# Optimization experiments

Measured on AMD Instinct MI355X. Metric: run time of the kernel, lower is better.

## Reference

```python
import jax, jax.numpy as jnp
import numpy as np

B, T, C, H, W = 4, 5, 512, 32, 32   # bt = B*T = 20
G = 32                              # GroupNorm groups
EPS = 1e-6


def group_norm(x, gamma, beta):
    # x: [N, C, H, W]; normalize per (group-channels, H, W)
    n, c, h, w = x.shape
    xg = x.reshape(n, G, c // G, h * w)
    mu = jnp.mean(xg, axis=(2, 3), keepdims=True)
    var = jnp.mean((xg - mu) ** 2, axis=(2, 3), keepdims=True)
    xn = ((xg - mu) * jax.lax.rsqrt(var + EPS)).reshape(n, c, h, w)
    return xn * gamma[None, :, None, None] + beta[None, :, None, None]


def conv1x1(x, w, b):
    # 1x1 conv == channel matmul. x: [N,C,H,W], w: [O,C], b: [O]
    return jnp.einsum('nchw,oc->nohw', x, w) + b[None, :, None, None]


def setup_inputs() -> dict:
    key = jax.random.key(0)
    ks = jax.random.split(key, 9)
    inp = {'x': jax.random.normal(ks[0], (B * T, C, H, W), jnp.float32)}
    for i, nm in enumerate(['wq', 'wk', 'wv', 'wo', 'wqt', 'wkt', 'wvt', 'wot']):
        inp[nm] = jax.random.normal(ks[i + 1], (C, C), jnp.float32) * 0.02
        inp['b' + nm[1:]] = jnp.zeros((C,), jnp.float32)
    inp['gamma_s'] = jnp.ones((C,), jnp.float32)
    inp['beta_s'] = jnp.zeros((C,), jnp.float32)
    inp['gamma_t'] = jnp.ones((C,), jnp.float32)
    inp['beta_t'] = jnp.zeros((C,), jnp.float32)
    return inp


def reference(x, wq, bq, wk, bk, wv, bv, wo, bo,
              wqt, bqt, wkt, bkt, wvt, bvt, wot, bot,
              gamma_s, beta_s, gamma_t, beta_t):
    scale = float(C) ** -0.5

    # ---- spatial attention (AttnBlock.forward) ----
    hn = group_norm(x, gamma_s, beta_s)
    q = conv1x1(hn, wq, bq).reshape(B * T, C, H * W)
    k = conv1x1(hn, wk, bk).reshape(B * T, C, H * W)
    v = conv1x1(hn, wv, bv).reshape(B * T, C, H * W)
    # scores [bt, hw_q, hw_k], softmax over keys
    att = jax.nn.softmax(jnp.einsum('bcq,bck->bqk', q, k) * scale, axis=2)
    hsp = jnp.einsum('bck,bqk->bcq', v, att).reshape(B * T, C, H, W)
    spatio = x + conv1x1(hsp, wo, bo)

    # ---- temporal attention across t=5 frames per pixel ----
    hn = group_norm(spatio, gamma_t, beta_t)
    q5 = conv1x1(hn, wqt, bqt).reshape(B, T, C, H, W)
    k5 = conv1x1(hn, wkt, bkt).reshape(B, T, C, H, W)
    v5 = conv1x1(hn, wvt, bvt).reshape(B, T, C, H, W)
    # per-pixel [t, t] attention, softmax over key-frame axis s
    att_t = jax.nn.softmax(jnp.einsum('btchw,bschw->bhwts', q5, k5) * scale, axis=-1)
    htp = jnp.einsum('bhwts,bschw->btchw', att_t, v5).reshape(B * T, C, H, W)

    # NOTE: residual is the ORIGINAL x (faithful to the source), not spatio
    return x + conv1x1(htp, wot, bot)
```

## Files before the change

kernel.cpp:

```cpp
#include <hip/hip_runtime.h>
#include <hip/hip_bf16.h>
#include <stdint.h>

typedef unsigned short u16;
typedef __attribute__((ext_vector_type(8))) short bf16x8;
typedef __attribute__((ext_vector_type(4))) float f32x4;

#define DI __device__ __forceinline__

DI float b2f(u16 u) { return __uint_as_float(((uint32_t)u) << 16); }
DI u16 f2b(float f) {
  uint32_t u = __float_as_uint(f);
  u += 0x7fff + ((u >> 16) & 1);
  return (u16)(u >> 16);
}

DI void gld_lds16(const u16* g, u16* l) {
  __builtin_amdgcn_global_load_lds((const __attribute__((address_space(1))) void*)g,
                                   (__attribute__((address_space(3))) void*)l,
                                   16, 0, 0);
}

__global__ __launch_bounds__(256)
void prep(const float* __restrict__ x, const float* __restrict__ gamma,
          const float* __restrict__ beta, u16* __restrict__ gnout,
          const float* __restrict__ w0, const float* __restrict__ w1,
          const float* __restrict__ w2, const float* __restrict__ w3,
          const float* __restrict__ w4, const float* __restrict__ w5,
          const float* __restrict__ w6, const float* __restrict__ w7,
          const float* __restrict__ b0, const float* __restrict__ b1,
          const float* __restrict__ b2, const float* __restrict__ b3,
          const float* __restrict__ b4, const float* __restrict__ b5,
          const float* __restrict__ b6, const float* __restrict__ b7,
          u16* __restrict__ dst, float* __restrict__ bdst)
{
  const int t = threadIdx.x;
  if (blockIdx.x < 640) {
    const int w = (blockIdx.x & 7) * 80 + (blockIdx.x >> 3);
    const int n = w >> 5, g = w & 31;
    const int C = 512, HW = 1024;
    const float* xg = x + ((long)n * C + g * 16) * HW;
    float s = 0.f, ss = 0.f;
    for (int ch = t; ch < 4096; ch += 256) {
      float4 u = *(const float4*)(xg + ch * 4);
      s += u.x + u.y + u.z + u.w;
      ss += u.x * u.x + u.y * u.y + u.z * u.z + u.w * u.w;
    }
#pragma unroll
    for (int off = 32; off > 0; off >>= 1) { s += __shfl_xor(s, off); ss += __shfl_xor(ss, off); }
    __shared__ float rs[4], rss[4];
    if ((t & 63) == 0) { rs[t >> 6] = s; rss[t >> 6] = ss; }
    __syncthreads();
    s  = rs[0] + rs[1] + rs[2] + rs[3];
    ss = rss[0] + rss[1] + rss[2] + rss[3];
    const float mu = s * (1.f / 16384.f);
    const float var = ss * (1.f / 16384.f) - mu * mu;
    const float rstd = rsqrtf(var + 1e-6f);
    float gm[16], bt[16];
#pragma unroll
    for (int i = 0; i < 16; ++i) {
      float ga = gamma[g * 16 + i];
      gm[i] = ga * rstd;
      bt[i] = beta[g * 16 + i] - mu * ga * rstd;
    }
    for (int p = t; p < 1024; p += 256) {
      alignas(16) u16 vals[16];
#pragma unroll
      for (int i = 0; i < 16; ++i)
        vals[i] = f2b(xg[(long)i * HW + p] * gm[i] + bt[i]);
      u16* dp = gnout + ((long)n * HW + p) * C + g * 16;
      *(uint4*)dp       = *(const uint4*)&vals[0];
      *(uint4*)(dp + 8) = *(const uint4*)&vals[8];
    }
    return;
  }
  const int sb = blockIdx.x - 640;
  if (sb >= 1036) {
    bdst[8192 + (sb - 1036) * 256 + t] = 0.f;
    return;
  }
  if (sb >= 1034) {
    const int a = (sb - 1034) * 256 + t;
    float acc = 0.f;
    for (int c = 0; c < 512; ++c) acc += w7[a * 512 + c] * b6[c];
    bdst[4608 + a] = acc + b7[a];
    return;
  }
  if (sb >= 1032) {
    const int a = (sb - 1032) * 256 + t;
    float acc = 0.f;
    for (int c = 0; c < 512; ++c) acc += w3[a * 512 + c] * b2[c];
    bdst[4096 + a] = acc;
    return;
  }
  if (sb >= 1024) {
    const float* bs8[8] = {b0, b1, b2, b3, b4, b5, b6, b7};
    const int a = sb - 1024;
    bdst[a * 512 + t] = bs8[a][t];
    bdst[a * 512 + t + 256] = bs8[a][t + 256];
    return;
  }
  const float* srcs[8] = {w0, w1, w2, w3, w4, w5, w6, w7};
  const int mat = sb >> 7;
  const int i = (((sb & 127) << 8) + t) * 8;
  const float* s = srcs[mat];
  float4 a = *(const float4*)(s + i);
  float4 b = *(const float4*)(s + i + 4);
  alignas(16) u16 v[8] = {f2b(a.x), f2b(a.y), f2b(a.z), f2b(a.w),
                          f2b(b.x), f2b(b.y), f2b(b.z), f2b(b.w)};
  *(uint4*)(dst + (long)mat * 262144 + i) = *(const uint4*)v;
  if (mat == 2 || mat == 6) {
    const int slot = (mat == 2) ? 8 : 10;
    const int row = i >> 9, col = i & 511;
#pragma unroll
    for (int j = 0; j < 8; ++j) dst[(long)slot * 262144 + (col + j) * 512 + row] = v[j];
  }
}

template<int OUTF32, int BIASMODE, int RESID, int SMEXP, int COLSCALE>
DI void gemm_body(const u16* __restrict__ Ab, long lda,
                  const u16* __restrict__ Bb, long ldb,
                  void* __restrict__ C, long cb,
                  const float* __restrict__ bias,
                  const float* __restrict__ resid, long rb,
                  int N, int K, float alpha,
                  float* __restrict__ stats, long stb,
                  int m0, int n0, u16* lA, u16* lB)
{
  const int t = threadIdx.x;
  const int lane = t & 63;
  const int wid = t >> 6;
  const int row = t >> 2;
  const int kc  = (((t & 3) ^ ((t >> 3) & 3)) << 3);

  f32x4 acc[4][4];
#pragma unroll
  for (int i = 0; i < 4; ++i)
#pragma unroll
    for (int j = 0; j < 4; ++j) acc[i][j] = (f32x4){0.f, 0.f, 0.f, 0.f};

  const int ml = lane & 15, qd = lane >> 4;
  const int koff = ((qd ^ ((ml >> 1) & 3)) << 3);
  const int wm = (wid >> 1) * 64, wn = (wid & 1) * 64;

  auto stage = [&](int bsel, int k0) {
    const u16* Ap = Ab + (long)(m0 + row) * lda + (k0 + kc);
    const u16* Bp = Bb + (long)(n0 + row) * ldb + (k0 + kc);
    u16* la = lA + bsel * 4096 + wid * 512;
    u16* lb = lB + bsel * 4096 + wid * 512;
    gld_lds16(Ap, la);
    gld_lds16(Ap + 64 * lda, la + 2048);
    gld_lds16(Bp, lb);
    gld_lds16(Bp + 64 * ldb, lb + 2048);
  };

  const int niter = K >> 5;
  stage(0, 0);
  for (int i = 0; i < niter; ++i) {
    __syncthreads();
    if (i + 1 < niter) stage((i + 1) & 1, (i + 1) << 5);
    const u16* la = lA + (i & 1) * 4096;
    const u16* lb = lB + (i & 1) * 4096;
    bf16x8 af[4], bfr[4];
#pragma unroll
    for (int x = 0; x < 4; ++x)
      af[x] = *(const bf16x8*)&la[(wm + x * 16 + ml) * 32 + koff];
#pragma unroll
    for (int y = 0; y < 4; ++y)
      bfr[y] = *(const bf16x8*)&lb[(wn + y * 16 + ml) * 32 + koff];
#pragma unroll
    for (int x = 0; x < 4; ++x)
#pragma unroll
      for (int y = 0; y < 4; ++y)
        acc[x][y] = __builtin_amdgcn_mfma_f32_16x16x32_bf16(af[x], bfr[y], acc[x][y], 0, 0, 0);
  }

  float inv[4], bcol[4];
  if (COLSCALE) {
#pragma unroll
    for (int j = 0; j < 4; ++j)
      inv[j] = 1.f / stats[stb + n0 + wn + j * 16 + ml];
  }
  if (BIASMODE == 2) {
#pragma unroll
    for (int j = 0; j < 4; ++j) bcol[j] = bias[n0 + wn + j * 16 + ml];
  }
  if (SMEXP) {
    float rs[16];
#pragma unroll
    for (int s = 0; s < 16; ++s) rs[s] = 0.f;
#pragma unroll
    for (int i = 0; i < 4; ++i)
#pragma unroll
      for (int j = 0; j < 4; ++j)
#pragma unroll
        for (int r2 = 0; r2 < 4; ++r2) {
          float e = __expf(acc[i][j][r2] * alpha);
          acc[i][j][r2] = e;
          rs[i * 4 + r2] += e;
        }
#pragma unroll
    for (int m = 1; m < 16; m <<= 1)
#pragma unroll
      for (int s = 0; s < 16; ++s) rs[s] += __shfl_xor(rs[s], m);
    if (ml == 0) {
#pragma unroll
      for (int i = 0; i < 4; ++i)
#pragma unroll
        for (int r2 = 0; r2 < 4; ++r2)
          atomicAdd(&stats[stb + m0 + wm + i * 16 + qd * 4 + r2], rs[i * 4 + r2]);
    }
  }

#pragma unroll
  for (int i = 0; i < 4; ++i) {
#pragma unroll
    for (int r2 = 0; r2 < 4; ++r2) {
      const int rr = m0 + wm + i * 16 + qd * 4 + r2;
      const float brow = (BIASMODE == 1) ? bias[rr] : 0.f;
      const long base = (long)rr * N + n0 + wn + ml;
#pragma unroll
      for (int j = 0; j < 4; ++j) {
        float v = acc[i][j][r2];
        if (!SMEXP) v *= alpha;
        if (COLSCALE) v *= inv[j];
        if (BIASMODE == 1) v += brow;
        if (BIASMODE == 2) v += bcol[j];
        const long ix = base + j * 16;
        if (RESID) v += resid[rb + ix];
        if (OUTF32) ((float*)C)[cb + ix] = v;
        else        ((u16*)C)[cb + ix] = f2b(v);
      }
    }
  }
}

template<int OUTF32, int BIASMODE, int RESID, int SMEXP, int COLSCALE>
__global__ __launch_bounds__(256)
void gemm_bt(const u16* __restrict__ A, long sA, long lda,
             const u16* __restrict__ B, long sB, long ldb,
             void* __restrict__ C, long sC,
             const float* __restrict__ bias,
             const float* __restrict__ resid, long sR,
             int N, int K, float alpha, float* __restrict__ stats)
{
  __shared__ u16 lA[2 * 128 * 32];
  __shared__ u16 lB[2 * 128 * 32];
  const uint32_t nx = gridDim.x, ny = gridDim.y;
  const uint32_t tpz = nx * ny;
  const uint32_t nblk = tpz * gridDim.z;
  const uint32_t g = ((uint32_t)blockIdx.z * ny + blockIdx.y) * nx + blockIdx.x;
  const uint32_t idx = (g & 7u) * (nblk >> 3) + (g >> 3);
  const uint32_t bz = idx / tpz;
  const uint32_t r   = idx - bz * tpz;
  const int m0 = (int)(r / nx) * 128, n0 = (int)(r % nx) * 128;
  gemm_body<OUTF32, BIASMODE, RESID, SMEXP, COLSCALE>(
      A + bz * sA, lda, B + bz * sB, ldb, C, bz * sC, bias, resid, bz * sR,
      N, K, alpha, stats, (long)bz * 1024, m0, n0, lA, lB);
}

__global__ __launch_bounds__(256)
void gemm_qkvv(const u16* __restrict__ hn, const u16* __restrict__ Wqk,
               u16* __restrict__ qkout, const float* __restrict__ bqk,
               const u16* __restrict__ Wov, u16* __restrict__ vvout,
               const float* __restrict__ bvv)
{
  __shared__ u16 lA[2 * 128 * 32];
  __shared__ u16 lB[2 * 128 * 32];
  const long S = 524288;
  const uint32_t g = blockIdx.x;
  if (g < 1280) {
    const uint32_t idx = (g & 7u) * 160 + (g >> 3);
    const int m0 = (int)(idx >> 3) * 128, n0 = (int)(idx & 7u) * 128;
    gemm_body<0, 2, 0, 0, 0>(hn, 512, Wqk, 512, qkout, 0, bqk, nullptr, 0,
                             1024, 512, 1.f, nullptr, 0, m0, n0, lA, lB);
  } else {
    const uint32_t gg = g - 1280;
    const uint32_t idx = (gg & 7u) * 80 + (gg >> 3);
    const uint32_t bz = idx >> 5;
    const uint32_t r = idx & 31u;
    const int m0 = (int)(r >> 3) * 128, n0 = (int)(r & 7u) * 128;
    gemm_body<0, 1, 0, 0, 0>(Wov, 512, hn + (long)bz * S, 512, vvout,
                             (long)bz * S, bvv, nullptr, 0,
                             1024, 512, 1.f, nullptr, 0, m0, n0, lA, lB);
  }
}

__global__ __launch_bounds__(256)
void groupnorm_resid(const u16* __restrict__ h, const float* __restrict__ x,
                     const float* __restrict__ gamma,
                     const float* __restrict__ beta, u16* __restrict__ out)
{
  const int C = 512, HW = 1024;
  const int w = (blockIdx.x & 7) * 80 + (blockIdx.x >> 3);
  const int n = w >> 5, g = w & 31;
  const long base = ((long)n * C + g * 16) * HW;
  const float* xg = x + base;
  const u16*  hg = h + base;
  const int t = threadIdx.x;
  float s = 0.f, ss = 0.f;
  for (int ch = t; ch < 4096; ch += 256) {
    float4 u = *(const float4*)(xg + ch * 4);
    uint2 hv = *(const uint2*)(hg + ch * 4);
    float h0 = __uint_as_float(hv.x << 16);
    float h1 = __uint_as_float(hv.x & 0xffff0000u);
    float h2 = __uint_as_float(hv.y << 16);
    float h3 = __uint_as_float(hv.y & 0xffff0000u);
    float v0 = u.x + h0, v1 = u.y + h1, v2 = u.z + h2, v3 = u.w + h3;
    s += v0 + v1 + v2 + v3;
    ss += v0 * v0 + v1 * v1 + v2 * v2 + v3 * v3;
  }
#pragma unroll
  for (int off = 32; off > 0; off >>= 1) { s += __shfl_xor(s, off); ss += __shfl_xor(ss, off); }
  __shared__ float rs[4], rss[4];
  if ((t & 63) == 0) { rs[t >> 6] = s; rss[t >> 6] = ss; }
  __syncthreads();
  s  = rs[0] + rs[1] + rs[2] + rs[3];
  ss = rss[0] + rss[1] + rss[2] + rss[3];
  const float mu = s * (1.f / 16384.f);
  const float var = ss * (1.f / 16384.f) - mu * mu;
  const float rstd = rsqrtf(var + 1e-6f);
  float gm[16], bt[16];
#pragma unroll
  for (int i = 0; i < 16; ++i) {
    float ga = gamma[g * 16 + i];
    gm[i] = ga * rstd;
    bt[i] = beta[g * 16 + i] - mu * ga * rstd;
  }
  for (int p = t; p < 1024; p += 256) {
    alignas(16) u16 vals[16];
#pragma unroll
    for (int i = 0; i < 16; ++i)
      vals[i] = f2b((xg[(long)i * HW + p] + b2f(hg[(long)i * HW + p])) * gm[i] + bt[i]);
    u16* dst = out + ((long)n * HW + p) * C + g * 16;
    *(uint4*)dst       = *(const uint4*)&vals[0];
    *(uint4*)(dst + 8) = *(const uint4*)&vals[8];
  }
}

__global__ __launch_bounds__(256)
void temporal_attn(const u16* __restrict__ qk, const u16* __restrict__ hn,
                   u16* __restrict__ htp)
{
  const int t = threadIdx.x;
  const int wv = t >> 6, lane = t & 63;
  const int pix = blockIdx.x * 4 + wv;
  const int b = pix >> 10, p = pix & 1023;
  const long fsq = 1024l * 1024;
  const long rowq = ((long)b * 5 * 1024 + p) * 1024 + lane * 8;
  const long fsh = 1024l * 512;
  const long rowh = ((long)b * 5 * 1024 + p) * 512 + lane * 8;

  float qf[5][8], kf[5][8];
#pragma unroll
  for (int f = 0; f < 5; ++f) {
    bf16x8 qv = *(const bf16x8*)(qk + rowq + f * fsq);
    bf16x8 kv = *(const bf16x8*)(qk + rowq + f * fsq + 512);
#pragma unroll
    for (int u = 0; u < 8; ++u) { qf[f][u] = b2f((u16)qv[u]); kf[f][u] = b2f((u16)kv[u]); }
  }
  float sc[25];
#pragma unroll
  for (int i = 0; i < 5; ++i)
#pragma unroll
    for (int j = 0; j < 5; ++j) {
      float a = 0.f;
#pragma unroll
      for (int u = 0; u < 8; ++u) a += qf[i][u] * kf[j][u];
      sc[i * 5 + j] = a;
    }
#pragma unroll
  for (int m = 1; m < 64; m <<= 1)
#pragma unroll
    for (int s = 0; s < 25; ++s) sc[s] += __shfl_xor(sc[s], m);

  const float scale = 0.04419417382415922f;
  float att[5][5];
#pragma unroll
  for (int i = 0; i < 5; ++i) {
    float m = sc[i * 5];
#pragma unroll
    for (int j = 1; j < 5; ++j) m = fmaxf(m, sc[i * 5 + j]);
    float ssum = 0.f;
#pragma unroll
    for (int j = 0; j < 5; ++j) { att[i][j] = __expf((sc[i * 5 + j] - m) * scale); ssum += att[i][j]; }
    float inv = 1.f / ssum;
#pragma unroll
    for (int j = 0; j < 5; ++j) att[i][j] *= inv;
  }

  float of[5][8];
#pragma unroll
  for (int i = 0; i < 5; ++i)
#pragma unroll
    for (int u = 0; u < 8; ++u) of[i][u] = 0.f;
#pragma unroll
  for (int s = 0; s < 5; ++s) {
    bf16x8 vvv = *(const bf16x8*)(hn + rowh + s * fsh);
#pragma unroll
    for (int u = 0; u < 8; ++u) {
      float vf = b2f((u16)vvv[u]);
#pragma unroll
      for (int i = 0; i < 5; ++i) of[i][u] += att[i][s] * vf;
    }
  }
#pragma unroll
  for (int i = 0; i < 5; ++i) {
    alignas(16) u16 ob[8];
#pragma unroll
    for (int u = 0; u < 8; ++u) ob[u] = f2b(of[i][u]);
    *(uint4*)(htp + rowh + i * fsh) = *(const uint4*)ob;
  }
}

extern "C" void kernel_launch(void* const* d_in, const int* in_sizes, int n_in,
                              void* d_out, int out_size, void* d_ws, size_t ws_size,
                              hipStream_t stream)
{
  const float* x   = (const float*)d_in[0];
  const float* wq  = (const float*)d_in[1];
  const float* bq  = (const float*)d_in[2];
  const float* wk  = (const float*)d_in[3];
  const float* bk  = (const float*)d_in[4];
  const float* wv  = (const float*)d_in[5];
  const float* bv  = (const float*)d_in[6];
  const float* wo  = (const float*)d_in[7];
  const float* bo  = (const float*)d_in[8];
  const float* wqt = (const float*)d_in[9];
  const float* bqt = (const float*)d_in[10];
  const float* wkt = (const float*)d_in[11];
  const float* bkt = (const float*)d_in[12];
  const float* wvt = (const float*)d_in[13];
  const float* bvt = (const float*)d_in[14];
  const float* wot = (const float*)d_in[15];
  const float* bot = (const float*)d_in[16];
  const float* gs  = (const float*)d_in[17];
  const float* bs  = (const float*)d_in[18];
  const float* gt  = (const float*)d_in[19];
  const float* btt = (const float*)d_in[20];

  const long U = 20l * 1024 * 512;
  u16* W0 = (u16*)d_ws;
  u16* W1 = W0 + U;
  u16* W3 = W0 + 3 * U;
  u16* W4 = W0 + 4 * U;
  u16* W6 = W0 + 6 * U;
  u16* W7 = W0 + 7 * U;
  u16* Wt = W0 + 8 * U;
  u16* wvT_b  = Wt + 8 * 262144;
  u16* Wovs   = Wt + 9 * 262144;
  u16* Wovt_b = Wt + 11 * 262144;
  float* Bf = (float*)(Wt + 12 * 262144);
  float* Stats = Bf + 8192;
  u16* wo_b  = Wt + 3 * 262144;
  u16* wqt_b = Wt + 4 * 262144;

  const long S  = 524288;
  const long S2 = 1048576;
  const float scale = 0.04419417382415922f;
  dim3 blk(256);

  prep<<<1756, blk, 0, stream>>>(x, gs, bs, W0,
                                 wq, wk, wv, wo, wqt, wkt, wvt, wot,
                                 bq, bk, bv, bo, bqt, bkt, bvt, bot, Wt, Bf);

  gemm_bt<0, 0, 0, 0, 0><<<dim3(4, 4, 2), blk, 0, stream>>>(
      wo_b, 4 * 262144, 512, wvT_b, 2 * 262144, 512, Wovs, 2 * 262144,
      nullptr, nullptr, 0, 512, 512, 1.f, nullptr);

  gemm_qkvv<<<1920, blk, 0, stream>>>(W0, Wt, W1, Bf, Wovs, W3, Bf + 4096);

  gemm_bt<0, 0, 0, 1, 0><<<dim3(8, 8, 20), blk, 0, stream>>>(
      W1, S2, 1024, W1 + 512, S2, 1024, W4, S2, nullptr, nullptr, 0, 1024, 512, scale, Stats);
  gemm_bt<0, 1, 0, 0, 1><<<dim3(8, 4, 20), blk, 0, stream>>>(
      W3, S, 1024, W4, S2, 1024, W6, S, Bf + 1536, nullptr, 0, 1024, 1024, 1.f, Stats);
  groupnorm_resid<<<640, blk, 0, stream>>>(W6, x, gt, btt, W7);
  gemm_bt<0, 2, 0, 0, 0><<<dim3(8, 160, 1), blk, 0, stream>>>(
      W7, 0, 512, wqt_b, 0, 512, W1, 0, Bf + 2048, nullptr, 0, 1024, 512, 1.f, nullptr);
  temporal_attn<<<1024, blk, 0, stream>>>(W1, W7, W0);
  gemm_bt<1, 1, 1, 0, 0><<<dim3(8, 4, 20), blk, 0, stream>>>(
      Wovt_b, 0, 512, W0, S, 512, (float*)d_out, S, Bf + 4608, x, S, 1024, 512, 1.f, nullptr);
}
```

Measured before the change: 390.4 us.

## Fold Wq/Wk into a single bilinear matrix for spatial and temporal scores

Replaces separate Q and K projections with one projection by a precomputed Wq^T·Wk product, so scores become hn·(M·hn) plus a key-side bias term from Wk^T·bq. The query-side bias terms cancel under the row softmax and are dropped. This halves the projection GEMM output width for both attention stages, and temporal attention reuses hn as both query and value inputs. The cost is an extra small weight-product GEMM, per-row bias dot products, and a modest change in bf16 rounding behaviour.

```diff
diff --git a/kernel.cpp b/kernel.cpp
--- a/kernel.cpp
+++ b/kernel.cpp
@@ -75,8 +75,22 @@
     return;
   }
   const int sb = blockIdx.x - 640;
+  if (sb >= 1040) {
+    bdst[8192 + (sb - 1040) * 256 + t] = 0.f;
+    return;
+  }
+  if (sb >= 1038) {
+    const int d = (sb - 1038) * 256 + t;
+    float acc = 0.f;
+    for (int e = 0; e < 512; ++e) acc += w5[(long)e * 512 + d] * b4[e];
+    bdst[5632 + d] = acc;
+    return;
+  }
   if (sb >= 1036) {
-    bdst[8192 + (sb - 1036) * 256 + t] = 0.f;
+    const int d = (sb - 1036) * 256 + t;
+    float acc = 0.f;
+    for (int e = 0; e < 512; ++e) acc += w1[(long)e * 512 + d] * b0[e];
+    bdst[5120 + d] = acc;
     return;
   }
   if (sb >= 1034) {
@@ -109,15 +123,16 @@
   alignas(16) u16 v[8] = {f2b(a.x), f2b(a.y), f2b(a.z), f2b(a.w),
                           f2b(b.x), f2b(b.y), f2b(b.z), f2b(b.w)};
   *(uint4*)(dst + (long)mat * 262144 + i) = *(const uint4*)v;
-  if (mat == 2 || mat == 6) {
-    const int slot = (mat == 2) ? 8 : 10;
+  const int tmap[8] = {11, 16, 8, -1, 15, 20, 12, -1};
+  const int ts = tmap[mat];
+  if (ts >= 0) {
     const int row = i >> 9, col = i & 511;
 #pragma unroll
-    for (int j = 0; j < 8; ++j) dst[(long)slot * 262144 + (col + j) * 512 + row] = v[j];
-  }
-}
-
-template<int OUTF32, int BIASMODE, int RESID, int SMEXP, int COLSCALE>
+    for (int j = 0; j < 8; ++j) dst[(long)ts * 262144 + (col + j) * 512 + row] = v[j];
+  }
+}
+
+template<int OUTF32, int BIASMODE, int RESID, int SMEXP, int COLSCALE, int COLB>
 DI void gemm_body(const u16* __restrict__ Ab, long lda,
                   const u16* __restrict__ Bb, long ldb,
                   void* __restrict__ C, long cb,
@@ -125,6 +140,7 @@
                   const float* __restrict__ resid, long rb,
                   int N, int K, float alpha,
                   float* __restrict__ stats, long stb,
+                  const float* __restrict__ cbias, long cbb,
                   int m0, int n0, u16* lA, u16* lB)
 {
   const int t = threadIdx.x;
@@ -175,7 +191,7 @@
         acc[x][y] = __builtin_amdgcn_mfma_f32_16x16x32_bf16(af[x], bfr[y], acc[x][y], 0, 0, 0);
   }
 
-  float inv[4], bcol[4];
+  float inv[4], bcol[4], cbl[4];
   if (COLSCALE) {
 #pragma unroll
     for (int j = 0; j < 4; ++j)
@@ -185,6 +201,10 @@
 #pragma unroll
     for (int j = 0; j < 4; ++j) bcol[j] = bias[n0 + wn + j * 16 + ml];
   }
+  if (COLB) {
+#pragma unroll
+    for (int j = 0; j < 4; ++j) cbl[j] = cbias[cbb + n0 + wn + j * 16 + ml];
+  }
   if (SMEXP) {
     float rs[16];
 #pragma unroll
@@ -195,7 +215,9 @@
       for (int j = 0; j < 4; ++j)
 #pragma unroll
         for (int r2 = 0; r2 < 4; ++r2) {
-          float e = __expf(acc[i][j][r2] * alpha);
+          float sv = acc[i][j][r2];
+          if (COLB) sv += cbl[j];
+          float e = __expf(sv * alpha);
           acc[i][j][r2] = e;
           rs[i * 4 + r2] += e;
         }
@@ -235,14 +257,15 @@
   }
 }
 
-template<int OUTF32, int BIASMODE, int RESID, int SMEXP, int COLSCALE>
+template<int OUTF32, int BIASMODE, int RESID, int SMEXP, int COLSCALE, int COLB>
 __global__ __launch_bounds__(256)
 void gemm_bt(const u16* __restrict__ A, long sA, long lda,
              const u16* __restrict__ B, long sB, long ldb,
              void* __restrict__ C, long sC,
              const float* __restrict__ bias,
              const float* __restrict__ resid, long sR,
-             int N, int K, float alpha, float* __restrict__ stats)
+             int N, int K, float alpha, float* __restrict__ stats,
+             const float* __restrict__ cbias)
 {
   __shared__ u16 lA[2 * 128 * 32];
   __shared__ u16 lB[2 * 128 * 32];
@@ -254,35 +277,56 @@
   const uint32_t bz = idx / tpz;
   const uint32_t r   = idx - bz * tpz;
   const int m0 = (int)(r / nx) * 128, n0 = (int)(r % nx) * 128;
-  gemm_body<OUTF32, BIASMODE, RESID, SMEXP, COLSCALE>(
+  gemm_body<OUTF32, BIASMODE, RESID, SMEXP, COLSCALE, COLB>(
       A + bz * sA, lda, B + bz * sB, ldb, C, bz * sC, bias, resid, bz * sR,
-      N, K, alpha, stats, (long)bz * 1024, m0, n0, lA, lB);
+      N, K, alpha, stats, (long)bz * 1024, cbias, (long)bz * 1024,
+      m0, n0, lA, lB);
 }
 
 __global__ __launch_bounds__(256)
-void gemm_qkvv(const u16* __restrict__ hn, const u16* __restrict__ Wqk,
-               u16* __restrict__ qkout, const float* __restrict__ bqk,
+void gemm_mkvv(const u16* __restrict__ hn, const u16* __restrict__ Ms,
+               u16* __restrict__ mkout,
                const u16* __restrict__ Wov, u16* __restrict__ vvout,
-               const float* __restrict__ bvv)
+               const float* __restrict__ bvv,
+               const float* __restrict__ ws, float* __restrict__ colt)
 {
   __shared__ u16 lA[2 * 128 * 32];
   __shared__ u16 lB[2 * 128 * 32];
   const long S = 524288;
+  const int t = threadIdx.x;
   const uint32_t g = blockIdx.x;
-  if (g < 1280) {
-    const uint32_t idx = (g & 7u) * 160 + (g >> 3);
-    const int m0 = (int)(idx >> 3) * 128, n0 = (int)(idx & 7u) * 128;
-    gemm_body<0, 2, 0, 0, 0>(hn, 512, Wqk, 512, qkout, 0, bqk, nullptr, 0,
-                             1024, 512, 1.f, nullptr, 0, m0, n0, lA, lB);
-  } else {
-    const uint32_t gg = g - 1280;
+  if (g < 640) {
+    const uint32_t idx = (g & 7u) * 80 + (g >> 3);
+    const int m0 = (int)(idx >> 2) * 128, n0 = (int)(idx & 3u) * 128;
+    gemm_body<0, 0, 0, 0, 0, 0>(hn, 512, Ms, 512, mkout, 0, nullptr,
+                                nullptr, 0, 512, 512, 1.f, nullptr, 0,
+                                nullptr, 0, m0, n0, lA, lB);
+  } else if (g < 1280) {
+    const uint32_t gg = g - 640;
     const uint32_t idx = (gg & 7u) * 80 + (gg >> 3);
     const uint32_t bz = idx >> 5;
     const uint32_t r = idx & 31u;
     const int m0 = (int)(r >> 3) * 128, n0 = (int)(r & 7u) * 128;
-    gemm_body<0, 1, 0, 0, 0>(Wov, 512, hn + (long)bz * S, 512, vvout,
-                             (long)bz * S, bvv, nullptr, 0,
-                             1024, 512, 1.f, nullptr, 0, m0, n0, lA, lB);
+    gemm_body<0, 1, 0, 0, 0, 0>(Wov, 512, hn + (long)bz * S, 512, vvout,
+                                (long)bz * S, bvv, nullptr, 0,
+                                1024, 512, 1.f, nullptr, 0, nullptr, 0,
+                                m0, n0, lA, lB);
+  } else {
+    const uint32_t gg = g - 1280;
+    const int lane = t & 63, wv = t >> 6;
+    float wsv[8];
+#pragma unroll
+    for (int u = 0; u < 8; ++u) wsv[u] = ws[lane * 8 + u];
+    for (int rr = 0; rr < 64; ++rr) {
+      const int row = gg * 256 + wv * 64 + rr;
+      bf16x8 hv = *(const bf16x8*)(hn + (long)row * 512 + lane * 8);
+      float a = 0.f;
+#pragma unroll
+      for (int u = 0; u < 8; ++u) a += b2f((u16)hv[u]) * wsv[u];
+#pragma unroll
+      for (int off = 32; off > 0; off >>= 1) a += __shfl_xor(a, off);
+      if (lane == 0) colt[row] = a;
+    }
   }
 }
 
@@ -339,27 +383,29 @@
 }
 
 __global__ __launch_bounds__(256)
-void temporal_attn(const u16* __restrict__ qk, const u16* __restrict__ hn,
-                   u16* __restrict__ htp)
+void temporal_attn(const u16* __restrict__ mkt, const u16* __restrict__ hn,
+                   u16* __restrict__ htp, const float* __restrict__ wt)
 {
   const int t = threadIdx.x;
   const int wv = t >> 6, lane = t & 63;
   const int pix = blockIdx.x * 4 + wv;
   const int b = pix >> 10, p = pix & 1023;
-  const long fsq = 1024l * 1024;
-  const long rowq = ((long)b * 5 * 1024 + p) * 1024 + lane * 8;
   const long fsh = 1024l * 512;
   const long rowh = ((long)b * 5 * 1024 + p) * 512 + lane * 8;
 
+  float wtv[8];
+#pragma unroll
+  for (int u = 0; u < 8; ++u) wtv[u] = wt[lane * 8 + u];
+
   float qf[5][8], kf[5][8];
 #pragma unroll
   for (int f = 0; f < 5; ++f) {
-    bf16x8 qv = *(const bf16x8*)(qk + rowq + f * fsq);
-    bf16x8 kv = *(const bf16x8*)(qk + rowq + f * fsq + 512);
+    bf16x8 qv = *(const bf16x8*)(hn  + rowh + f * fsh);
+    bf16x8 kv = *(const bf16x8*)(mkt + rowh + f * fsh);
 #pragma unroll
     for (int u = 0; u < 8; ++u) { qf[f][u] = b2f((u16)qv[u]); kf[f][u] = b2f((u16)kv[u]); }
   }
-  float sc[25];
+  float sc[30];
 #pragma unroll
   for (int i = 0; i < 5; ++i)
 #pragma unroll
@@ -370,20 +416,30 @@
       sc[i * 5 + j] = a;
     }
 #pragma unroll
+  for (int f = 0; f < 5; ++f) {
+    float a = 0.f;
+#pragma unroll
+    for (int u = 0; u < 8; ++u) a += qf[f][u] * wtv[u];
+    sc[25 + f] = a;
+  }
+#pragma unroll
   for (int m = 1; m < 64; m <<= 1)
 #pragma unroll
-    for (int s = 0; s < 25; ++s) sc[s] += __shfl_xor(sc[s], m);
+    for (int s = 0; s < 30; ++s) sc[s] += __shfl_xor(sc[s], m);
 
   const float scale = 0.04419417382415922f;
   float att[5][5];
 #pragma unroll
   for (int i = 0; i < 5; ++i) {
-    float m = sc[i * 5];
-#pragma unroll
-    for (int j = 1; j < 5; ++j) m = fmaxf(m, sc[i * 5 + j]);
+    float sf[5];
+#pragma unroll
+    for (int j = 0; j < 5; ++j) sf[j] = sc[i * 5 + j] + sc[25 + j];
+    float m = sf[0];
+#pragma unroll
+    for (int j = 1; j < 5; ++j) m = fmaxf(m, sf[j]);
     float ssum = 0.f;
 #pragma unroll
-    for (int j = 0; j < 5; ++j) { att[i][j] = __expf((sc[i * 5 + j] - m) * scale); ssum += att[i][j]; }
+    for (int j = 0; j < 5; ++j) { att[i][j] = __expf((sf[j] - m) * scale); ssum += att[i][j]; }
     float inv = 1.f / ssum;
 #pragma unroll
     for (int j = 0; j < 5; ++j) att[i][j] *= inv;
@@ -395,15 +451,13 @@
 #pragma unroll
     for (int u = 0; u < 8; ++u) of[i][u] = 0.f;
 #pragma unroll
-  for (int s = 0; s < 5; ++s) {
-    bf16x8 vvv = *(const bf16x8*)(hn + rowh + s * fsh);
+  for (int s = 0; s < 5; ++s)
 #pragma unroll
     for (int u = 0; u < 8; ++u) {
-      float vf = b2f((u16)vvv[u]);
+      const float vf = qf[s][u];
 #pragma unroll
       for (int i = 0; i < 5; ++i) of[i][u] += att[i][s] * vf;
     }
-  }
 #pragma unroll
   for (int i = 0; i < 5; ++i) {
     alignas(16) u16 ob[8];
@@ -447,37 +501,46 @@
   u16* W6 = W0 + 6 * U;
   u16* W7 = W0 + 7 * U;
   u16* Wt = W0 + 8 * U;
+  u16* wo_b   = Wt + 3 * 262144;
   u16* wvT_b  = Wt + 8 * 262144;
   u16* Wovs   = Wt + 9 * 262144;
-  u16* Wovt_b = Wt + 11 * 262144;
-  float* Bf = (float*)(Wt + 12 * 262144);
+  u16* Wovt_b = Wt + 13 * 262144;
+  u16* Ms_b   = Wt + 17 * 262144;
+  u16* Mt_b   = Wt + 21 * 262144;
+  float* Bf = (float*)(Wt + 22 * 262144);
+  float* Ws_v = Bf + 5120;
+  float* Wt_v = Bf + 5632;
   float* Stats = Bf + 8192;
-  u16* wo_b  = Wt + 3 * 262144;
-  u16* wqt_b = Wt + 4 * 262144;
+  float* Colt  = Bf + 28672;
 
   const long S  = 524288;
   const long S2 = 1048576;
   const float scale = 0.04419417382415922f;
   dim3 blk(256);
 
-  prep<<<1756, blk, 0, stream>>>(x, gs, bs, W0,
+  prep<<<1760, blk, 0, stream>>>(x, gs, bs, W0,
                                  wq, wk, wv, wo, wqt, wkt, wvt, wot,
                                  bq, bk, bv, bo, bqt, bkt, bvt, bot, Wt, Bf);
 
-  gemm_bt<0, 0, 0, 0, 0><<<dim3(4, 4, 2), blk, 0, stream>>>(
-      wo_b, 4 * 262144, 512, wvT_b, 2 * 262144, 512, Wovs, 2 * 262144,
-      nullptr, nullptr, 0, 512, 512, 1.f, nullptr);
-
-  gemm_qkvv<<<1920, blk, 0, stream>>>(W0, Wt, W1, Bf, Wovs, W3, Bf + 4096);
-
-  gemm_bt<0, 0, 0, 1, 0><<<dim3(8, 8, 20), blk, 0, stream>>>(
-      W1, S2, 1024, W1 + 512, S2, 1024, W4, S2, nullptr, nullptr, 0, 1024, 512, scale, Stats);
-  gemm_bt<0, 1, 0, 0, 1><<<dim3(8, 4, 20), blk, 0, stream>>>(
-      W3, S, 1024, W4, S2, 1024, W6, S, Bf + 1536, nullptr, 0, 1024, 1024, 1.f, Stats);
+  gemm_bt<0, 0, 0, 0, 0, 0><<<dim3(4, 4, 4), blk, 0, stream>>>(
+      wo_b, 4 * 262144, 512, wvT_b, 4 * 262144, 512, Wovs, 4 * 262144,
+      nullptr, nullptr, 0, 512, 512, 1.f, nullptr, nullptr);
+
+  gemm_mkvv<<<1360, blk, 0, stream>>>(W0, Ms_b, W1, Wovs, W3, Bf + 4096,
+                                      Ws_v, Colt);
+
+  gemm_bt<0, 0, 0, 1, 0, 1><<<dim3(8, 8, 20), blk, 0, stream>>>(
+      W0, S, 512, W1, S, 512, W4, S2, nullptr, nullptr, 0,
+      1024, 512, scale, Stats, Colt);
+  gemm_bt<0, 1, 0, 0, 1, 0><<<dim3(8, 4, 20), blk, 0, stream>>>(
+      W3, S, 1024, W4, S2, 1024, W6, S, Bf + 1536, nullptr, 0,
+      1024, 1024, 1.f, Stats, nullptr);
   groupnorm_resid<<<640, blk, 0, stream>>>(W6, x, gt, btt, W7);
-  gemm_bt<0, 2, 0, 0, 0><<<dim3(8, 160, 1), blk, 0, stream>>>(
-      W7, 0, 512, wqt_b, 0, 512, W1, 0, Bf + 2048, nullptr, 0, 1024, 512, 1.f, nullptr);
-  temporal_attn<<<1024, blk, 0, stream>>>(W1, W7, W0);
-  gemm_bt<1, 1, 1, 0, 0><<<dim3(8, 4, 20), blk, 0, stream>>>(
-      Wovt_b, 0, 512, W0, S, 512, (float*)d_out, S, Bf + 4608, x, S, 1024, 512, 1.f, nullptr);
-}
+  gemm_bt<0, 0, 0, 0, 0, 0><<<dim3(4, 160, 1), blk, 0, stream>>>(
+      W7, 0, 512, Mt_b, 0, 512, W1, 0, nullptr, nullptr, 0,
+      512, 512, 1.f, nullptr, nullptr);
+  temporal_attn<<<1024, blk, 0, stream>>>(W1, W7, W0, Wt_v);
+  gemm_bt<1, 1, 1, 0, 0, 0><<<dim3(8, 4, 20), blk, 0, stream>>>(
+      Wovt_b, 0, 512, W0, S, 512, (float*)d_out, S, Bf + 4608, x, S,
+      1024, 512, 1.f, nullptr, nullptr);
+}
```

Result: no change. 393.2 us (+0.7%).
